# Kernel optimization log

Measured on AMD Instinct MI355X. Metric: run time of the kernel, lower is better.

## Reference

```python
import jax, jax.numpy as jnp
import numpy as np

IMG_C = 256
GC = 32  # graph_channel; must equal graph feature dim 32 for the residual


def setup_inputs() -> dict:
    key = jax.random.key(0)
    ks = jax.random.split(key, 10)
    B, N, WH_SIDE = 8, 4096, 64
    s = lambda fan_in: 1.0 / np.sqrt(fan_in)
    return {
        "input_graph": jax.random.normal(ks[0], (B, N, GC), jnp.float32),
        "input_image": jax.random.normal(ks[1], (B, IMG_C, WH_SIDE, WH_SIDE), jnp.float32),
        # Conv1d(kernel=1) weights stored as [out, in]
        "Wq": jax.random.uniform(ks[2], (GC, 32), jnp.float32, -s(32), s(32)),
        "bq": jax.random.uniform(ks[3], (GC,), jnp.float32, -s(32), s(32)),
        "Wk": jax.random.uniform(ks[4], (GC, IMG_C), jnp.float32, -s(IMG_C), s(IMG_C)),
        "bk": jax.random.uniform(ks[5], (GC,), jnp.float32, -s(IMG_C), s(IMG_C)),
        "Wv": jax.random.uniform(ks[6], (GC, IMG_C), jnp.float32, -s(IMG_C), s(IMG_C)),
        "bv": jax.random.uniform(ks[7], (GC,), jnp.float32, -s(IMG_C), s(IMG_C)),
        "Wc": jax.random.uniform(ks[8], (GC, GC), jnp.float32, -s(GC), s(GC)),
        "bc": jax.random.uniform(ks[9], (GC,), jnp.float32, -s(GC), s(GC)),
    }


def reference(input_graph, input_image, Wq, bq, Wk, bk, Wv, bv, Wc, bc):
    B, C, W, H = input_image.shape
    img = input_image.reshape(B, C, W * H)                      # [B, C, L]
    # 1x1 conv projections == channel matmuls
    K = jnp.einsum('oc,bcl->bol', Wk, img) + bk[None, :, None]  # [B, GC, L]
    V = jnp.einsum('oc,bcl->bol', Wv, img) + bv[None, :, None]  # [B, GC, L]
    # Q: graph [B, N, 32] -> conv over channel dim -> [B, N, GC]
    Q = jnp.einsum('oc,bnc->bno', Wq, input_graph) + bq[None, None, :]
    att = jnp.einsum('bno,bol->bnl', Q, K) / jnp.sqrt(jnp.float32(GC))  # [B, N, L]
    # NOTE: original softmax is over dim=1 (the node/query axis)
    att = jax.nn.softmax(att, axis=1)
    message = jnp.einsum('bol,bnl->bon', V, att)                # [B, GC, N]
    out = input_graph.transpose(0, 2, 1) + (
        jnp.einsum('oc,bcn->bon', Wc, message) + bc[None, :, None]
    )                                                           # [B, GC, N]
    return out.transpose(0, 2, 1)                               # [B, N, GC]
```

## Files before the change

### kernel.cpp

```cpp
#include <hip/hip_runtime.h>

#define BB 8
#define NN 4096
#define LL 4096
#define CC 256

typedef short bf16x8 __attribute__((ext_vector_type(8)));
typedef _Float16 f16x8 __attribute__((ext_vector_type(8)));
typedef __fp16 hf16x2 __attribute__((ext_vector_type(2)));
typedef float f32x4 __attribute__((ext_vector_type(4)));

__device__ __forceinline__ short f2bf(float f) {
  union { float f; unsigned u; } v; v.f = f;
  unsigned r = v.u + 0x7fffu + ((v.u >> 16) & 1u);
  return (short)(r >> 16);
}
__device__ __forceinline__ bf16x8 ld8(const float* __restrict__ fp) {
  float4 a = *(const float4*)fp;
  float4 b = *(const float4*)(fp + 4);
  bf16x8 r;
  r[0] = f2bf(a.x); r[1] = f2bf(a.y); r[2] = f2bf(a.z); r[3] = f2bf(a.w);
  r[4] = f2bf(b.x); r[5] = f2bf(b.y); r[6] = f2bf(b.z); r[7] = f2bf(b.w);
  return r;
}

__global__ __launch_bounds__(256) void ka_proj(
    const float* __restrict__ graph, const float* __restrict__ img,
    const float* __restrict__ Wq, const float* __restrict__ bq,
    const float* __restrict__ Wk, const float* __restrict__ bk,
    const float* __restrict__ Wv, const float* __restrict__ bv,
    short* __restrict__ Qb, short* __restrict__ Kt, _Float16* __restrict__ Vt,
    float* __restrict__ Zbuf)
{
  const int tid = threadIdx.x;
  const int w = tid >> 6, lane = tid & 63, lo = lane & 15, q = lane >> 4;
  const int bid = blockIdx.x;
  if (bid < 512) {
    const int b = bid >> 6;
    if (tid < 64) Zbuf[(size_t)b * LL + ((bid & 63) << 6) + tid] = 0.0f;
    const int lt = ((bid & 63) << 6) + (w << 4);
    f32x4 aK0 = {0,0,0,0}, aK1 = {0,0,0,0}, aV0 = {0,0,0,0}, aV1 = {0,0,0,0};
    const float* ib = img + (size_t)b * CC * LL + lt + lo;
    #pragma unroll
    for (int cs = 0; cs < 8; ++cs) {
      const int c0 = cs * 32 + q * 8;
      bf16x8 bi;
      #pragma unroll
      for (int j = 0; j < 8; ++j) bi[j] = f2bf(ib[(size_t)(c0 + j) * LL]);
      bf16x8 wk0 = ld8(Wk + lo * CC + c0);
      bf16x8 wk1 = ld8(Wk + (lo + 16) * CC + c0);
      bf16x8 wv0 = ld8(Wv + lo * CC + c0);
      bf16x8 wv1 = ld8(Wv + (lo + 16) * CC + c0);
      aK0 = __builtin_amdgcn_mfma_f32_16x16x32_bf16(wk0, bi, aK0, 0, 0, 0);
      aK1 = __builtin_amdgcn_mfma_f32_16x16x32_bf16(wk1, bi, aK1, 0, 0, 0);
      aV0 = __builtin_amdgcn_mfma_f32_16x16x32_bf16(wv0, bi, aV0, 0, 0, 0);
      aV1 = __builtin_amdgcn_mfma_f32_16x16x32_bf16(wv1, bi, aV1, 0, 0, 0);
    }
    const float kscale = 0.2550348663f;
    const size_t row = ((size_t)b * LL + lt + lo) * 32;
    short4 s0, s1;
    s0.x = f2bf((aK0[0] + bk[q * 4 + 0]) * kscale);
    s0.y = f2bf((aK0[1] + bk[q * 4 + 1]) * kscale);
    s0.z = f2bf((aK0[2] + bk[q * 4 + 2]) * kscale);
    s0.w = f2bf((aK0[3] + bk[q * 4 + 3]) * kscale);
    s1.x = f2bf((aK1[0] + bk[16 + q * 4 + 0]) * kscale);
    s1.y = f2bf((aK1[1] + bk[16 + q * 4 + 1]) * kscale);
    s1.z = f2bf((aK1[2] + bk[16 + q * 4 + 2]) * kscale);
    s1.w = f2bf((aK1[3] + bk[16 + q * 4 + 3]) * kscale);
    *(short4*)(Kt + row + q * 4) = s0;
    *(short4*)(Kt + row + 16 + q * 4) = s1;
    union { hf16x2 h[2]; uint2 u; } p0, p1;
    p0.h[0] = __builtin_amdgcn_cvt_pkrtz(aV0[0] + bv[q * 4 + 0], aV0[1] + bv[q * 4 + 1]);
    p0.h[1] = __builtin_amdgcn_cvt_pkrtz(aV0[2] + bv[q * 4 + 2], aV0[3] + bv[q * 4 + 3]);
    p1.h[0] = __builtin_amdgcn_cvt_pkrtz(aV1[0] + bv[16 + q * 4 + 0], aV1[1] + bv[16 + q * 4 + 1]);
    p1.h[1] = __builtin_amdgcn_cvt_pkrtz(aV1[2] + bv[16 + q * 4 + 2], aV1[3] + bv[16 + q * 4 + 3]);
    *(uint2*)(Vt + row + q * 4) = p0.u;
    *(uint2*)(Vt + row + 16 + q * 4) = p1.u;
  } else {
    const int t = bid - 512;
    const int b = t >> 6;
    const int nt = ((t & 63) << 6) + (w << 4);
    bf16x8 ag = ld8(graph + ((size_t)b * NN + nt + lo) * 32 + q * 8);
    bf16x8 w0 = ld8(Wq + lo * 32 + q * 8);
    bf16x8 w1 = ld8(Wq + (lo + 16) * 32 + q * 8);
    f32x4 z = {0,0,0,0};
    f32x4 a0 = __builtin_amdgcn_mfma_f32_16x16x32_bf16(ag, w0, z, 0, 0, 0);
    f32x4 a1 = __builtin_amdgcn_mfma_f32_16x16x32_bf16(ag, w1, z, 0, 0, 0);
    const float b0 = bq[lo], b1 = bq[lo + 16];
    #pragma unroll
    for (int r = 0; r < 4; ++r) {
      const size_t rowq = ((size_t)b * NN + nt + q * 4 + r) * 32;
      Qb[rowq + lo] = f2bf(a0[r] + b0);
      Qb[rowq + 16 + lo] = f2bf(a1[r] + b1);
    }
  }
}

__global__ __launch_bounds__(256) void kb1_z(
    const short* __restrict__ Qb, const short* __restrict__ Kt,
    float* __restrict__ Z)
{
  const int tid = threadIdx.x;
  const int w = tid >> 6, lane = tid & 63, lo = lane & 15, q = lane >> 4;
  const int bid = blockIdx.x;
  const int b = bid >> 8;
  const int l0 = ((bid >> 2) & 63) << 6;
  const int nq = bid & 3;
  bf16x8 kf[4];
  #pragma unroll
  for (int f = 0; f < 4; ++f)
    kf[f] = *(const bf16x8*)(Kt + ((size_t)b * LL + l0 + f * 16 + lo) * 32 + q * 8);
  float za[4][4] = {{0}};
  const short* qbase = Qb + ((size_t)b * NN + nq * 1024 + w * 256 + lo) * 32 + q * 8;
  #pragma unroll 4
  for (int it = 0; it < 16; ++it) {
    bf16x8 qf = *(const bf16x8*)(qbase + it * 512);
    #pragma unroll
    for (int f = 0; f < 4; ++f) {
      f32x4 z = {0,0,0,0};
      f32x4 c = __builtin_amdgcn_mfma_f32_16x16x32_bf16(kf[f], qf, z, 0, 0, 0);
      #pragma unroll
      for (int r = 0; r < 4; ++r) za[f][r] += __builtin_amdgcn_exp2f(c[r]);
    }
  }
  #pragma unroll
  for (int m = 1; m < 16; m <<= 1)
    #pragma unroll
    for (int f = 0; f < 4; ++f)
      #pragma unroll
      for (int r = 0; r < 4; ++r)
        za[f][r] += __shfl_xor(za[f][r], m, 64);
  if (lo == 0) {
    #pragma unroll
    for (int f = 0; f < 4; ++f)
      #pragma unroll
      for (int r = 0; r < 4; ++r)
        atomicAdd(&Z[(size_t)b * LL + l0 + f * 16 + q * 4 + r], za[f][r]);
  }
}

__global__ __launch_bounds__(256) void kb2_scale(
    const _Float16* __restrict__ Vt, const float* __restrict__ Z,
    _Float16* __restrict__ Vpp)
{
  const int tid = threadIdx.x;
  const int b = blockIdx.x >> 6;
  const int l = ((blockIdx.x & 63) << 6) + (tid & 63);
  const int og = tid >> 6;
  const float inv = __builtin_amdgcn_rcpf(Z[(size_t)b * LL + l]) * 4096.0f;
  const f16x8 vv = *(const f16x8*)(Vt + ((size_t)b * LL + l) * 32 + og * 8);
  #pragma unroll
  for (int j = 0; j < 8; ++j)
    Vpp[((size_t)b * 32 + og * 8 + j) * LL + l] = (_Float16)((float)vv[j] * inv);
}

__global__ __launch_bounds__(256) void kc_attn(
    const short* __restrict__ Qb, const short* __restrict__ Kt,
    const _Float16* __restrict__ Vpp, const float* __restrict__ graph,
    const float* __restrict__ Wc, const float* __restrict__ bc,
    float* __restrict__ out)
{
  __shared__ __align__(16) unsigned char smem[4 * 32 * 72 * 2];
  const int tid = threadIdx.x;
  const int w = tid >> 6, lane = tid & 63, lo = lane & 15, q = lane >> 4;
  const int b = blockIdx.x >> 7;
  const int n0 = (blockIdx.x & 127) << 5;
  _Float16* Pw = (_Float16*)smem + w * (32 * 72);
  float* MS = (float*)smem;
  const bf16x8 qf0 = *(const bf16x8*)(Qb + ((size_t)b * NN + n0 + lo) * 32 + q * 8);
  const bf16x8 qf1 = *(const bf16x8*)(Qb + ((size_t)b * NN + n0 + 16 + lo) * 32 + q * 8);
  f32x4 m00 = {0,0,0,0}, m01 = {0,0,0,0}, m10 = {0,0,0,0}, m11 = {0,0,0,0};
  const short* ktb = Kt + (size_t)b * LL * 32 + lo * 32 + q * 8;
  const _Float16* vb0 = Vpp + ((size_t)b * 32 + lo) * LL;
  const _Float16* vb1 = vb0 + (size_t)16 * LL;
  const int lc0 = w * 16;
  bf16x8 kfN[4];
  #pragma unroll
  for (int f = 0; f < 4; ++f)
    kfN[f] = *(const bf16x8*)(ktb + (size_t)(lc0 * 64 + f * 16) * 32);
  for (int lc = lc0; lc < lc0 + 16; ++lc) {
    const int lbase = lc * 64;
    bf16x8 kfC[4];
    #pragma unroll
    for (int f = 0; f < 4; ++f) kfC[f] = kfN[f];
    f16x8 vA0 = *(const f16x8*)(vb0 + lbase + q * 8);
    f16x8 vA1 = *(const f16x8*)(vb0 + lbase + 32 + q * 8);
    f16x8 vB0 = *(const f16x8*)(vb1 + lbase + q * 8);
    f16x8 vB1 = *(const f16x8*)(vb1 + lbase + 32 + q * 8);
    const int lcn = (lc + 1 < lc0 + 16) ? lc + 1 : lc;
    #pragma unroll
    for (int f = 0; f < 4; ++f)
      kfN[f] = *(const bf16x8*)(ktb + (size_t)(lcn * 64 + f * 16) * 32);
    #pragma unroll
    for (int f = 0; f < 4; ++f) {
      f32x4 z = {0,0,0,0};
      f32x4 c0 = __builtin_amdgcn_mfma_f32_16x16x32_bf16(kfC[f], qf0, z, 0, 0, 0);
      f32x4 c1 = __builtin_amdgcn_mfma_f32_16x16x32_bf16(kfC[f], qf1, z, 0, 0, 0);
      union { hf16x2 h[2]; uint2 u; } pk0, pk1;
      pk0.h[0] = __builtin_amdgcn_cvt_pkrtz(__builtin_amdgcn_exp2f(c0[0]),
                                            __builtin_amdgcn_exp2f(c0[1]));
      pk0.h[1] = __builtin_amdgcn_cvt_pkrtz(__builtin_amdgcn_exp2f(c0[2]),
                                            __builtin_amdgcn_exp2f(c0[3]));
      pk1.h[0] = __builtin_amdgcn_cvt_pkrtz(__builtin_amdgcn_exp2f(c1[0]),
                                            __builtin_amdgcn_exp2f(c1[1]));
      pk1.h[1] = __builtin_amdgcn_cvt_pkrtz(__builtin_amdgcn_exp2f(c1[2]),
                                            __builtin_amdgcn_exp2f(c1[3]));
      *(uint2*)&Pw[lo * 72 + f * 16 + q * 4] = pk0.u;
      *(uint2*)&Pw[(16 + lo) * 72 + f * 16 + q * 4] = pk1.u;
    }
    {
      f16x8 pa00 = *(const f16x8*)&Pw[lo * 72 + q * 8];
      f16x8 pa01 = *(const f16x8*)&Pw[lo * 72 + 32 + q * 8];
      f16x8 pa10 = *(const f16x8*)&Pw[(16 + lo) * 72 + q * 8];
      f16x8 pa11 = *(const f16x8*)&Pw[(16 + lo) * 72 + 32 + q * 8];
      m00 = __builtin_amdgcn_mfma_f32_16x16x32_f16(pa00, vA0, m00, 0, 0, 0);
      m10 = __builtin_amdgcn_mfma_f32_16x16x32_f16(pa10, vA0, m10, 0, 0, 0);
      m01 = __builtin_amdgcn_mfma_f32_16x16x32_f16(pa00, vB0, m01, 0, 0, 0);
      m11 = __builtin_amdgcn_mfma_f32_16x16x32_f16(pa10, vB0, m11, 0, 0, 0);
      m00 = __builtin_amdgcn_mfma_f32_16x16x32_f16(pa01, vA1, m00, 0, 0, 0);
      m10 = __builtin_amdgcn_mfma_f32_16x16x32_f16(pa11, vA1, m10, 0, 0, 0);
      m01 = __builtin_amdgcn_mfma_f32_16x16x32_f16(pa01, vB1, m01, 0, 0, 0);
      m11 = __builtin_amdgcn_mfma_f32_16x16x32_f16(pa11, vB1, m11, 0, 0, 0);
    }
  }
  float* MSw = MS + w * (32 * 36);
  #pragma unroll
  for (int r = 0; r < 4; ++r) {
    MSw[(q * 4 + r) * 36 + lo] = m00[r];
    MSw[(q * 4 + r) * 36 + 16 + lo] = m01[r];
    MSw[(16 + q * 4 + r) * 36 + lo] = m10[r];
    MSw[(16 + q * 4 + r) * 36 + 16 + lo] = m11[r];
  }
  __syncthreads();
  const int o = lane & 31, nh = lane >> 5;
  float wcr[32];
  #pragma unroll
  for (int c4 = 0; c4 < 8; ++c4) {
    float4 wc4 = *(const float4*)(Wc + o * 32 + c4 * 4);
    wcr[c4 * 4 + 0] = wc4.x * (1.0f / 4096.0f);
    wcr[c4 * 4 + 1] = wc4.y * (1.0f / 4096.0f);
    wcr[c4 * 4 + 2] = wc4.z * (1.0f / 4096.0f);
    wcr[c4 * 4 + 3] = wc4.w * (1.0f / 4096.0f);
  }
  const float bcv = bc[o];
  #pragma unroll
  for (int rr = 0; rr < 4; ++rr) {
    const int nl = w * 8 + nh * 4 + rr;
    f32x4 s = {0,0,0,0};
    #pragma unroll
    for (int cc = 0; cc < 8; ++cc) {
      f32x4 ma = *(const f32x4*)&MS[0 * 1152 + nl * 36 + cc * 4];
      f32x4 mb = *(const f32x4*)&MS[1 * 1152 + nl * 36 + cc * 4];
      f32x4 mc = *(const f32x4*)&MS[2 * 1152 + nl * 36 + cc * 4];
      f32x4 md = *(const f32x4*)&MS[3 * 1152 + nl * 36 + cc * 4];
      f32x4 m4 = ma + mb + mc + md;
      s[0] += wcr[cc * 4 + 0] * m4[0];
      s[1] += wcr[cc * 4 + 1] * m4[1];
      s[2] += wcr[cc * 4 + 2] * m4[2];
      s[3] += wcr[cc * 4 + 3] * m4[3];
    }
    const size_t idx = ((size_t)b * NN + n0 + nl) * 32 + o;
    out[idx] = s[0] + s[1] + s[2] + s[3] + bcv + graph[idx];
  }
}

extern "C" void kernel_launch(void* const* d_in, const int* in_sizes, int n_in,
                              void* d_out, int out_size, void* d_ws, size_t ws_size,
                              hipStream_t stream) {
  const float* graph = (const float*)d_in[0];
  const float* img   = (const float*)d_in[1];
  const float* Wq    = (const float*)d_in[2];
  const float* bq    = (const float*)d_in[3];
  const float* Wk    = (const float*)d_in[4];
  const float* bk    = (const float*)d_in[5];
  const float* Wv    = (const float*)d_in[6];
  const float* bv    = (const float*)d_in[7];
  const float* Wc    = (const float*)d_in[8];
  const float* bc    = (const float*)d_in[9];
  char* ws = (char*)d_ws;
  short*    Qb  = (short*)(ws + 0);
  short*    Kt  = (short*)(ws + 2097152);
  _Float16* Vt  = (_Float16*)(ws + 4194304);
  _Float16* Vpp = (_Float16*)(ws + 6291456);
  float*    Zb  = (float*)(ws + 8388608);
  ka_proj<<<dim3(1024), dim3(256), 0, stream>>>(graph, img, Wq, bq, Wk, bk, Wv, bv,
                                                Qb, Kt, Vt, Zb);
  kb1_z<<<dim3(2048), dim3(256), 0, stream>>>(Qb, Kt, Zb);
  kb2_scale<<<dim3(512), dim3(256), 0, stream>>>(Vt, Zb, Vpp);
  kc_attn<<<dim3(1024), dim3(256), 0, stream>>>(Qb, Kt, Vpp, graph, Wc, bc,
                                                (float*)d_out);
}
```

Before: 185.4 us.

## Software-pipeline attention loop with double-buffered P tiles across iterations

Restructures the main attention loop so that the P·V MFMAs for the previous L-chunk are issued after the QK/exp stage of the current chunk. The P tile in LDS is ping-ponged between two buffers, and V fragments are carried one iteration behind. This is meant to hide the LDS write-to-read latency and the exp work behind MFMA execution. LDS use per block doubles, the MS reduction offsets are adjusted to match, and launch bounds request 4 blocks per CU, which may constrain registers.

```diff
diff --git a/kernel.cpp b/kernel.cpp
--- a/kernel.cpp
+++ b/kernel.cpp
@@ -154,18 +154,67 @@
     Vpp[((size_t)b * 32 + og * 8 + j) * LL + l] = (_Float16)((float)vv[j] * inv);
 }
 
-__global__ __launch_bounds__(256) void kc_attn(
+#define KC_BODY(LC, PWR, PRD, DOPV)                                           \
+  {                                                                           \
+    const int lbase_ = (LC) * 64;                                             \
+    const int lcn_ = ((LC) + 1 < lc0 + 16) ? (LC) + 1 : (LC);                 \
+    bf16x8 kfN_[4];                                                           \
+    _Pragma("unroll")                                                         \
+    for (int f = 0; f < 4; ++f)                                               \
+      kfN_[f] = *(const bf16x8*)(ktb + (size_t)(lcn_ * 64 + f * 16) * 32);    \
+    f16x8 vN0_ = *(const f16x8*)(vb0 + lbase_ + q * 8);                       \
+    f16x8 vN1_ = *(const f16x8*)(vb0 + lbase_ + 32 + q * 8);                  \
+    f16x8 vN2_ = *(const f16x8*)(vb1 + lbase_ + q * 8);                       \
+    f16x8 vN3_ = *(const f16x8*)(vb1 + lbase_ + 32 + q * 8);                  \
+    _Pragma("unroll")                                                         \
+    for (int f = 0; f < 4; ++f) {                                             \
+      f32x4 z_ = {0, 0, 0, 0};                                                \
+      f32x4 c0_ = __builtin_amdgcn_mfma_f32_16x16x32_bf16(kfC[f], qf0, z_, 0, 0, 0); \
+      f32x4 c1_ = __builtin_amdgcn_mfma_f32_16x16x32_bf16(kfC[f], qf1, z_, 0, 0, 0); \
+      union { hf16x2 h[2]; uint2 u; } pk0_, pk1_;                             \
+      pk0_.h[0] = __builtin_amdgcn_cvt_pkrtz(__builtin_amdgcn_exp2f(c0_[0]),  \
+                                             __builtin_amdgcn_exp2f(c0_[1])); \
+      pk0_.h[1] = __builtin_amdgcn_cvt_pkrtz(__builtin_amdgcn_exp2f(c0_[2]),  \
+                                             __builtin_amdgcn_exp2f(c0_[3])); \
+      pk1_.h[0] = __builtin_amdgcn_cvt_pkrtz(__builtin_amdgcn_exp2f(c1_[0]),  \
+                                             __builtin_amdgcn_exp2f(c1_[1])); \
+      pk1_.h[1] = __builtin_amdgcn_cvt_pkrtz(__builtin_amdgcn_exp2f(c1_[2]),  \
+                                             __builtin_amdgcn_exp2f(c1_[3])); \
+      *(uint2*)&(PWR)[lo * 72 + f * 16 + q * 4] = pk0_.u;                     \
+      *(uint2*)&(PWR)[(16 + lo) * 72 + f * 16 + q * 4] = pk1_.u;              \
+    }                                                                         \
+    if (DOPV) {                                                               \
+      f16x8 pa00_ = *(const f16x8*)&(PRD)[lo * 72 + q * 8];                   \
+      f16x8 pa01_ = *(const f16x8*)&(PRD)[lo * 72 + 32 + q * 8];              \
+      f16x8 pa10_ = *(const f16x8*)&(PRD)[(16 + lo) * 72 + q * 8];            \
+      f16x8 pa11_ = *(const f16x8*)&(PRD)[(16 + lo) * 72 + 32 + q * 8];       \
+      m00 = __builtin_amdgcn_mfma_f32_16x16x32_f16(pa00_, vC0, m00, 0, 0, 0); \
+      m10 = __builtin_amdgcn_mfma_f32_16x16x32_f16(pa10_, vC0, m10, 0, 0, 0); \
+      m01 = __builtin_amdgcn_mfma_f32_16x16x32_f16(pa00_, vC2, m01, 0, 0, 0); \
+      m11 = __builtin_amdgcn_mfma_f32_16x16x32_f16(pa10_, vC2, m11, 0, 0, 0); \
+      m00 = __builtin_amdgcn_mfma_f32_16x16x32_f16(pa01_, vC1, m00, 0, 0, 0); \
+      m10 = __builtin_amdgcn_mfma_f32_16x16x32_f16(pa11_, vC1, m10, 0, 0, 0); \
+      m01 = __builtin_amdgcn_mfma_f32_16x16x32_f16(pa01_, vC3, m01, 0, 0, 0); \
+      m11 = __builtin_amdgcn_mfma_f32_16x16x32_f16(pa11_, vC3, m11, 0, 0, 0); \
+    }                                                                         \
+    vC0 = vN0_; vC1 = vN1_; vC2 = vN2_; vC3 = vN3_;                           \
+    _Pragma("unroll")                                                         \
+    for (int f = 0; f < 4; ++f) kfC[f] = kfN_[f];                             \
+  }
+
+__global__ __launch_bounds__(256, 4) void kc_attn(
     const short* __restrict__ Qb, const short* __restrict__ Kt,
     const _Float16* __restrict__ Vpp, const float* __restrict__ graph,
     const float* __restrict__ Wc, const float* __restrict__ bc,
     float* __restrict__ out)
 {
-  __shared__ __align__(16) unsigned char smem[4 * 32 * 72 * 2];
+  __shared__ __align__(16) unsigned char smem[4 * 2 * 32 * 72 * 2];
   const int tid = threadIdx.x;
   const int w = tid >> 6, lane = tid & 63, lo = lane & 15, q = lane >> 4;
   const int b = blockIdx.x >> 7;
   const int n0 = (blockIdx.x & 127) << 5;
-  _Float16* Pw = (_Float16*)smem + w * (32 * 72);
+  _Float16* PA = (_Float16*)smem + (w * 2 + 0) * (32 * 72);
+  _Float16* PB = (_Float16*)smem + (w * 2 + 1) * (32 * 72);
   float* MS = (float*)smem;
   const bf16x8 qf0 = *(const bf16x8*)(Qb + ((size_t)b * NN + n0 + lo) * 32 + q * 8);
   const bf16x8 qf1 = *(const bf16x8*)(Qb + ((size_t)b * NN + n0 + 16 + lo) * 32 + q * 8);
@@ -174,56 +223,33 @@
   const _Float16* vb0 = Vpp + ((size_t)b * 32 + lo) * LL;
   const _Float16* vb1 = vb0 + (size_t)16 * LL;
   const int lc0 = w * 16;
-  bf16x8 kfN[4];
+  bf16x8 kfC[4];
   #pragma unroll
   for (int f = 0; f < 4; ++f)
-    kfN[f] = *(const bf16x8*)(ktb + (size_t)(lc0 * 64 + f * 16) * 32);
-  for (int lc = lc0; lc < lc0 + 16; ++lc) {
-    const int lbase = lc * 64;
-    bf16x8 kfC[4];
-    #pragma unroll
-    for (int f = 0; f < 4; ++f) kfC[f] = kfN[f];
-    f16x8 vA0 = *(const f16x8*)(vb0 + lbase + q * 8);
-    f16x8 vA1 = *(const f16x8*)(vb0 + lbase + 32 + q * 8);
-    f16x8 vB0 = *(const f16x8*)(vb1 + lbase + q * 8);
-    f16x8 vB1 = *(const f16x8*)(vb1 + lbase + 32 + q * 8);
-    const int lcn = (lc + 1 < lc0 + 16) ? lc + 1 : lc;
-    #pragma unroll
-    for (int f = 0; f < 4; ++f)
-      kfN[f] = *(const bf16x8*)(ktb + (size_t)(lcn * 64 + f * 16) * 32);
-    #pragma unroll
-    for (int f = 0; f < 4; ++f) {
-      f32x4 z = {0,0,0,0};
-      f32x4 c0 = __builtin_amdgcn_mfma_f32_16x16x32_bf16(kfC[f], qf0, z, 0, 0, 0);
-      f32x4 c1 = __builtin_amdgcn_mfma_f32_16x16x32_bf16(kfC[f], qf1, z, 0, 0, 0);
-      union { hf16x2 h[2]; uint2 u; } pk0, pk1;
-      pk0.h[0] = __builtin_amdgcn_cvt_pkrtz(__builtin_amdgcn_exp2f(c0[0]),
-                                            __builtin_amdgcn_exp2f(c0[1]));
-      pk0.h[1] = __builtin_amdgcn_cvt_pkrtz(__builtin_amdgcn_exp2f(c0[2]),
-                                            __builtin_amdgcn_exp2f(c0[3]));
-      pk1.h[0] = __builtin_amdgcn_cvt_pkrtz(__builtin_amdgcn_exp2f(c1[0]),
-                                            __builtin_amdgcn_exp2f(c1[1]));
-      pk1.h[1] = __builtin_amdgcn_cvt_pkrtz(__builtin_amdgcn_exp2f(c1[2]),
-                                            __builtin_amdgcn_exp2f(c1[3]));
-      *(uint2*)&Pw[lo * 72 + f * 16 + q * 4] = pk0.u;
-      *(uint2*)&Pw[(16 + lo) * 72 + f * 16 + q * 4] = pk1.u;
-    }
-    {
-      f16x8 pa00 = *(const f16x8*)&Pw[lo * 72 + q * 8];
-      f16x8 pa01 = *(const f16x8*)&Pw[lo * 72 + 32 + q * 8];
-      f16x8 pa10 = *(const f16x8*)&Pw[(16 + lo) * 72 + q * 8];
-      f16x8 pa11 = *(const f16x8*)&Pw[(16 + lo) * 72 + 32 + q * 8];
-      m00 = __builtin_amdgcn_mfma_f32_16x16x32_f16(pa00, vA0, m00, 0, 0, 0);
-      m10 = __builtin_amdgcn_mfma_f32_16x16x32_f16(pa10, vA0, m10, 0, 0, 0);
-      m01 = __builtin_amdgcn_mfma_f32_16x16x32_f16(pa00, vB0, m01, 0, 0, 0);
-      m11 = __builtin_amdgcn_mfma_f32_16x16x32_f16(pa10, vB0, m11, 0, 0, 0);
-      m00 = __builtin_amdgcn_mfma_f32_16x16x32_f16(pa01, vA1, m00, 0, 0, 0);
-      m10 = __builtin_amdgcn_mfma_f32_16x16x32_f16(pa11, vA1, m10, 0, 0, 0);
-      m01 = __builtin_amdgcn_mfma_f32_16x16x32_f16(pa01, vB1, m01, 0, 0, 0);
-      m11 = __builtin_amdgcn_mfma_f32_16x16x32_f16(pa11, vB1, m11, 0, 0, 0);
-    }
-  }
-  float* MSw = MS + w * (32 * 36);
+    kfC[f] = *(const bf16x8*)(ktb + (size_t)(lc0 * 64 + f * 16) * 32);
+  f16x8 vC0 = {0,0,0,0,0,0,0,0}, vC1 = {0,0,0,0,0,0,0,0};
+  f16x8 vC2 = {0,0,0,0,0,0,0,0}, vC3 = {0,0,0,0,0,0,0,0};
+  #pragma unroll 1
+  for (int i2 = 0; i2 < 8; ++i2) {
+    const int lce = lc0 + i2 * 2;
+    KC_BODY(lce, PA, PB, (i2 != 0));
+    KC_BODY(lce + 1, PB, PA, true);
+  }
+  {
+    f16x8 pa00_ = *(const f16x8*)&PB[lo * 72 + q * 8];
+    f16x8 pa01_ = *(const f16x8*)&PB[lo * 72 + 32 + q * 8];
+    f16x8 pa10_ = *(const f16x8*)&PB[(16 + lo) * 72 + q * 8];
+    f16x8 pa11_ = *(const f16x8*)&PB[(16 + lo) * 72 + 32 + q * 8];
+    m00 = __builtin_amdgcn_mfma_f32_16x16x32_f16(pa00_, vC0, m00, 0, 0, 0);
+    m10 = __builtin_amdgcn_mfma_f32_16x16x32_f16(pa10_, vC0, m10, 0, 0, 0);
+    m01 = __builtin_amdgcn_mfma_f32_16x16x32_f16(pa00_, vC2, m01, 0, 0, 0);
+    m11 = __builtin_amdgcn_mfma_f32_16x16x32_f16(pa10_, vC2, m11, 0, 0, 0);
+    m00 = __builtin_amdgcn_mfma_f32_16x16x32_f16(pa01_, vC1, m00, 0, 0, 0);
+    m10 = __builtin_amdgcn_mfma_f32_16x16x32_f16(pa11_, vC1, m10, 0, 0, 0);
+    m01 = __builtin_amdgcn_mfma_f32_16x16x32_f16(pa01_, vC3, m01, 0, 0, 0);
+    m11 = __builtin_amdgcn_mfma_f32_16x16x32_f16(pa11_, vC3, m11, 0, 0, 0);
+  }
+  float* MSw = MS + w * 2304;
   #pragma unroll
   for (int r = 0; r < 4; ++r) {
     MSw[(q * 4 + r) * 36 + lo] = m00[r];
@@ -249,10 +275,10 @@
     f32x4 s = {0,0,0,0};
     #pragma unroll
     for (int cc = 0; cc < 8; ++cc) {
-      f32x4 ma = *(const f32x4*)&MS[0 * 1152 + nl * 36 + cc * 4];
-      f32x4 mb = *(const f32x4*)&MS[1 * 1152 + nl * 36 + cc * 4];
-      f32x4 mc = *(const f32x4*)&MS[2 * 1152 + nl * 36 + cc * 4];
-      f32x4 md = *(const f32x4*)&MS[3 * 1152 + nl * 36 + cc * 4];
+      f32x4 ma = *(const f32x4*)&MS[0 * 2304 + nl * 36 + cc * 4];
+      f32x4 mb = *(const f32x4*)&MS[1 * 2304 + nl * 36 + cc * 4];
+      f32x4 mc = *(const f32x4*)&MS[2 * 2304 + nl * 36 + cc * 4];
+      f32x4 md = *(const f32x4*)&MS[3 * 2304 + nl * 36 + cc * 4];
       f32x4 m4 = ma + mb + mc + md;
       s[0] += wcr[cc * 4 + 0] * m4[0];
       s[1] += wcr[cc * 4 + 1] * m4[1];
```

Result: no change. 183.4 us (-1.1%).

## Enlarge per-block tiles in Z-reduction and attention kernels for operand reuse

Applied to the files above, without the earlier changes.

kb1_z now has each block cover 128 L positions instead of 64, which halves the grid and doubles the reuse of each Q fragment. kc_attn now has each block cover 64 query nodes instead of 32, so each K and V fragment load is reused across four query tiles and K/V global traffic drops by half. Both kernels now map the batch index to the low bits of the block id. kc_attn drops the explicit next-iteration K prefetch, so K load latency may be exposed, and the larger tiles raise register and LDS use, which can lower occupancy on a smaller grid.

```diff
diff --git a/kernel.cpp b/kernel.cpp
--- a/kernel.cpp
+++ b/kernel.cpp
@@ -103,20 +103,21 @@
   const int tid = threadIdx.x;
   const int w = tid >> 6, lane = tid & 63, lo = lane & 15, q = lane >> 4;
   const int bid = blockIdx.x;
-  const int b = bid >> 8;
-  const int l0 = ((bid >> 2) & 63) << 6;
-  const int nq = bid & 3;
-  bf16x8 kf[4];
-  #pragma unroll
-  for (int f = 0; f < 4; ++f)
+  const int b = bid & 7;
+  const int t = bid >> 3;
+  const int l0 = (t >> 2) << 7;
+  const int nq = t & 3;
+  bf16x8 kf[8];
+  #pragma unroll
+  for (int f = 0; f < 8; ++f)
     kf[f] = *(const bf16x8*)(Kt + ((size_t)b * LL + l0 + f * 16 + lo) * 32 + q * 8);
-  float za[4][4] = {{0}};
+  float za[8][4] = {{0}};
   const short* qbase = Qb + ((size_t)b * NN + nq * 1024 + w * 256 + lo) * 32 + q * 8;
   #pragma unroll 4
   for (int it = 0; it < 16; ++it) {
     bf16x8 qf = *(const bf16x8*)(qbase + it * 512);
     #pragma unroll
-    for (int f = 0; f < 4; ++f) {
+    for (int f = 0; f < 8; ++f) {
       f32x4 z = {0,0,0,0};
       f32x4 c = __builtin_amdgcn_mfma_f32_16x16x32_bf16(kf[f], qf, z, 0, 0, 0);
       #pragma unroll
@@ -126,13 +127,13 @@
   #pragma unroll
   for (int m = 1; m < 16; m <<= 1)
     #pragma unroll
-    for (int f = 0; f < 4; ++f)
+    for (int f = 0; f < 8; ++f)
       #pragma unroll
       for (int r = 0; r < 4; ++r)
         za[f][r] += __shfl_xor(za[f][r], m, 64);
   if (lo == 0) {
     #pragma unroll
-    for (int f = 0; f < 4; ++f)
+    for (int f = 0; f < 8; ++f)
       #pragma unroll
       for (int r = 0; r < 4; ++r)
         atomicAdd(&Z[(size_t)b * LL + l0 + f * 16 + q * 4 + r], za[f][r]);
@@ -160,78 +161,69 @@
     const float* __restrict__ Wc, const float* __restrict__ bc,
     float* __restrict__ out)
 {
-  __shared__ __align__(16) unsigned char smem[4 * 32 * 72 * 2];
+  __shared__ __align__(16) unsigned char smem[4 * 9216];
   const int tid = threadIdx.x;
   const int w = tid >> 6, lane = tid & 63, lo = lane & 15, q = lane >> 4;
-  const int b = blockIdx.x >> 7;
-  const int n0 = (blockIdx.x & 127) << 5;
-  _Float16* Pw = (_Float16*)smem + w * (32 * 72);
-  float* MS = (float*)smem;
-  const bf16x8 qf0 = *(const bf16x8*)(Qb + ((size_t)b * NN + n0 + lo) * 32 + q * 8);
-  const bf16x8 qf1 = *(const bf16x8*)(Qb + ((size_t)b * NN + n0 + 16 + lo) * 32 + q * 8);
-  f32x4 m00 = {0,0,0,0}, m01 = {0,0,0,0}, m10 = {0,0,0,0}, m11 = {0,0,0,0};
+  const int b = blockIdx.x & 7;
+  const int n0 = ((int)blockIdx.x >> 3) << 6;
+  _Float16* Pw = (_Float16*)(smem + w * 9216);
+  bf16x8 qf[4];
+  #pragma unroll
+  for (int nq = 0; nq < 4; ++nq)
+    qf[nq] = *(const bf16x8*)(Qb + ((size_t)b * NN + n0 + nq * 16 + lo) * 32 + q * 8);
+  f32x4 m[4][2];
+  #pragma unroll
+  for (int nq = 0; nq < 4; ++nq) {
+    m[nq][0] = (f32x4){0,0,0,0};
+    m[nq][1] = (f32x4){0,0,0,0};
+  }
   const short* ktb = Kt + (size_t)b * LL * 32 + lo * 32 + q * 8;
   const _Float16* vb0 = Vpp + ((size_t)b * 32 + lo) * LL;
   const _Float16* vb1 = vb0 + (size_t)16 * LL;
   const int lc0 = w * 16;
-  bf16x8 kfN[4];
-  #pragma unroll
-  for (int f = 0; f < 4; ++f)
-    kfN[f] = *(const bf16x8*)(ktb + (size_t)(lc0 * 64 + f * 16) * 32);
   for (int lc = lc0; lc < lc0 + 16; ++lc) {
     const int lbase = lc * 64;
-    bf16x8 kfC[4];
-    #pragma unroll
-    for (int f = 0; f < 4; ++f) kfC[f] = kfN[f];
+    bf16x8 kf[4];
+    #pragma unroll
+    for (int f = 0; f < 4; ++f)
+      kf[f] = *(const bf16x8*)(ktb + (size_t)(lbase + f * 16) * 32);
     f16x8 vA0 = *(const f16x8*)(vb0 + lbase + q * 8);
     f16x8 vA1 = *(const f16x8*)(vb0 + lbase + 32 + q * 8);
     f16x8 vB0 = *(const f16x8*)(vb1 + lbase + q * 8);
     f16x8 vB1 = *(const f16x8*)(vb1 + lbase + 32 + q * 8);
-    const int lcn = (lc + 1 < lc0 + 16) ? lc + 1 : lc;
-    #pragma unroll
-    for (int f = 0; f < 4; ++f)
-      kfN[f] = *(const bf16x8*)(ktb + (size_t)(lcn * 64 + f * 16) * 32);
-    #pragma unroll
-    for (int f = 0; f < 4; ++f) {
-      f32x4 z = {0,0,0,0};
-      f32x4 c0 = __builtin_amdgcn_mfma_f32_16x16x32_bf16(kfC[f], qf0, z, 0, 0, 0);
-      f32x4 c1 = __builtin_amdgcn_mfma_f32_16x16x32_bf16(kfC[f], qf1, z, 0, 0, 0);
-      union { hf16x2 h[2]; uint2 u; } pk0, pk1;
-      pk0.h[0] = __builtin_amdgcn_cvt_pkrtz(__builtin_amdgcn_exp2f(c0[0]),
-                                            __builtin_amdgcn_exp2f(c0[1]));
-      pk0.h[1] = __builtin_amdgcn_cvt_pkrtz(__builtin_amdgcn_exp2f(c0[2]),
-                                            __builtin_amdgcn_exp2f(c0[3]));
-      pk1.h[0] = __builtin_amdgcn_cvt_pkrtz(__builtin_amdgcn_exp2f(c1[0]),
-                                            __builtin_amdgcn_exp2f(c1[1]));
-      pk1.h[1] = __builtin_amdgcn_cvt_pkrtz(__builtin_amdgcn_exp2f(c1[2]),
-                                            __builtin_amdgcn_exp2f(c1[3]));
-      *(uint2*)&Pw[lo * 72 + f * 16 + q * 4] = pk0.u;
-      *(uint2*)&Pw[(16 + lo) * 72 + f * 16 + q * 4] = pk1.u;
-    }
-    {
-      f16x8 pa00 = *(const f16x8*)&Pw[lo * 72 + q * 8];
-      f16x8 pa01 = *(const f16x8*)&Pw[lo * 72 + 32 + q * 8];
-      f16x8 pa10 = *(const f16x8*)&Pw[(16 + lo) * 72 + q * 8];
-      f16x8 pa11 = *(const f16x8*)&Pw[(16 + lo) * 72 + 32 + q * 8];
-      m00 = __builtin_amdgcn_mfma_f32_16x16x32_f16(pa00, vA0, m00, 0, 0, 0);
-      m10 = __builtin_amdgcn_mfma_f32_16x16x32_f16(pa10, vA0, m10, 0, 0, 0);
-      m01 = __builtin_amdgcn_mfma_f32_16x16x32_f16(pa00, vB0, m01, 0, 0, 0);
-      m11 = __builtin_amdgcn_mfma_f32_16x16x32_f16(pa10, vB0, m11, 0, 0, 0);
-      m00 = __builtin_amdgcn_mfma_f32_16x16x32_f16(pa01, vA1, m00, 0, 0, 0);
-      m10 = __builtin_amdgcn_mfma_f32_16x16x32_f16(pa11, vA1, m10, 0, 0, 0);
-      m01 = __builtin_amdgcn_mfma_f32_16x16x32_f16(pa01, vB1, m01, 0, 0, 0);
-      m11 = __builtin_amdgcn_mfma_f32_16x16x32_f16(pa11, vB1, m11, 0, 0, 0);
-    }
-  }
-  float* MSw = MS + w * (32 * 36);
-  #pragma unroll
-  for (int r = 0; r < 4; ++r) {
-    MSw[(q * 4 + r) * 36 + lo] = m00[r];
-    MSw[(q * 4 + r) * 36 + 16 + lo] = m01[r];
-    MSw[(16 + q * 4 + r) * 36 + lo] = m10[r];
-    MSw[(16 + q * 4 + r) * 36 + 16 + lo] = m11[r];
-  }
+    #pragma unroll
+    for (int nq = 0; nq < 4; ++nq)
+      #pragma unroll
+      for (int f = 0; f < 4; ++f) {
+        f32x4 z = {0,0,0,0};
+        f32x4 c = __builtin_amdgcn_mfma_f32_16x16x32_bf16(kf[f], qf[nq], z, 0, 0, 0);
+        union { hf16x2 h[2]; uint2 u; } pk;
+        pk.h[0] = __builtin_amdgcn_cvt_pkrtz(__builtin_amdgcn_exp2f(c[0]),
+                                             __builtin_amdgcn_exp2f(c[1]));
+        pk.h[1] = __builtin_amdgcn_cvt_pkrtz(__builtin_amdgcn_exp2f(c[2]),
+                                             __builtin_amdgcn_exp2f(c[3]));
+        *(uint2*)&Pw[(nq * 16 + lo) * 72 + f * 16 + q * 4] = pk.u;
+      }
+    #pragma unroll
+    for (int nq = 0; nq < 4; ++nq) {
+      f16x8 pa0 = *(const f16x8*)&Pw[(nq * 16 + lo) * 72 + q * 8];
+      f16x8 pa1 = *(const f16x8*)&Pw[(nq * 16 + lo) * 72 + 32 + q * 8];
+      m[nq][0] = __builtin_amdgcn_mfma_f32_16x16x32_f16(pa0, vA0, m[nq][0], 0, 0, 0);
+      m[nq][1] = __builtin_amdgcn_mfma_f32_16x16x32_f16(pa0, vB0, m[nq][1], 0, 0, 0);
+      m[nq][0] = __builtin_amdgcn_mfma_f32_16x16x32_f16(pa1, vA1, m[nq][0], 0, 0, 0);
+      m[nq][1] = __builtin_amdgcn_mfma_f32_16x16x32_f16(pa1, vB1, m[nq][1], 0, 0, 0);
+    }
+  }
+  float* MSw = (float*)(smem + w * 9216);
+  #pragma unroll
+  for (int nq = 0; nq < 4; ++nq)
+    #pragma unroll
+    for (int r = 0; r < 4; ++r) {
+      MSw[(nq * 16 + q * 4 + r) * 36 + lo] = m[nq][0][r];
+      MSw[(nq * 16 + q * 4 + r) * 36 + 16 + lo] = m[nq][1][r];
+    }
   __syncthreads();
+  const float* MS = (const float*)smem;
   const int o = lane & 31, nh = lane >> 5;
   float wcr[32];
   #pragma unroll
@@ -244,15 +236,15 @@
   }
   const float bcv = bc[o];
   #pragma unroll
-  for (int rr = 0; rr < 4; ++rr) {
-    const int nl = w * 8 + nh * 4 + rr;
+  for (int rr = 0; rr < 8; ++rr) {
+    const int nl = w * 16 + nh * 8 + rr;
     f32x4 s = {0,0,0,0};
     #pragma unroll
     for (int cc = 0; cc < 8; ++cc) {
-      f32x4 ma = *(const f32x4*)&MS[0 * 1152 + nl * 36 + cc * 4];
-      f32x4 mb = *(const f32x4*)&MS[1 * 1152 + nl * 36 + cc * 4];
-      f32x4 mc = *(const f32x4*)&MS[2 * 1152 + nl * 36 + cc * 4];
-      f32x4 md = *(const f32x4*)&MS[3 * 1152 + nl * 36 + cc * 4];
+      f32x4 ma = *(const f32x4*)&MS[0 * 2304 + nl * 36 + cc * 4];
+      f32x4 mb = *(const f32x4*)&MS[1 * 2304 + nl * 36 + cc * 4];
+      f32x4 mc = *(const f32x4*)&MS[2 * 2304 + nl * 36 + cc * 4];
+      f32x4 md = *(const f32x4*)&MS[3 * 2304 + nl * 36 + cc * 4];
       f32x4 m4 = ma + mb + mc + md;
       s[0] += wcr[cc * 4 + 0] * m4[0];
       s[1] += wcr[cc * 4 + 1] * m4[1];
@@ -285,8 +277,8 @@
   float*    Zb  = (float*)(ws + 8388608);
   ka_proj<<<dim3(1024), dim3(256), 0, stream>>>(graph, img, Wq, bq, Wk, bk, Wv, bv,
                                                 Qb, Kt, Vt, Zb);
-  kb1_z<<<dim3(2048), dim3(256), 0, stream>>>(Qb, Kt, Zb);
+  kb1_z<<<dim3(1024), dim3(256), 0, stream>>>(Qb, Kt, Zb);
   kb2_scale<<<dim3(512), dim3(256), 0, stream>>>(Vt, Zb, Vpp);
-  kc_attn<<<dim3(1024), dim3(256), 0, stream>>>(Qb, Kt, Vpp, graph, Wc, bc,
-                                                (float*)d_out);
-}
+  kc_attn<<<dim3(512), dim3(256), 0, stream>>>(Qb, Kt, Vpp, graph, Wc, bc,
+                                               (float*)d_out);
+}
```

Measured after the change: 175.9 us. 1.05x faster.
